# Optimization experiments

Hardware: AMD Instinct MI355X
Metric: run time of the kernel (lower is better)

## Reference

```python
import jax, jax.numpy as jnp
import numpy as np

TOP_K = 2  # num_experts_per_token


def setup_inputs() -> dict:
    key = jax.random.key(0)
    ks = jax.random.split(key, 6)
    B, S, H, F, E = 4, 2048, 1024, 4096, 8  # F = 2 * intermediate_size
    scale = 0.02
    x = jax.random.normal(ks[0], (B, S, H), dtype=jnp.float32)
    gate_w = jax.random.normal(ks[1], (E, H), dtype=jnp.float32) * scale
    w1 = jax.random.normal(ks[2], (E, H, F), dtype=jnp.float32) * scale
    b1 = jnp.zeros((E, F), dtype=jnp.float32)
    w2 = jax.random.normal(ks[3], (E, F, H), dtype=jnp.float32) * scale
    b2 = jnp.zeros((E, H), dtype=jnp.float32)
    return {"x": x, "gate_w": gate_w, "w1": w1, "b1": b1, "w2": w2, "b2": b2}


def reference(x, gate_w, w1, b1, w2, b2):
    # x: [B, S, H]; gate_w: [E, H]; w1: [E, H, F]; b1: [E, F]; w2: [E, F, H]; b2: [E, H]
    E = gate_w.shape[0]
    gate_logits = jnp.einsum('bsh,eh->bse', x, gate_w)
    gate_probs = jax.nn.softmax(gate_logits, axis=-1)
    top_v, top_i = jax.lax.top_k(gate_probs, TOP_K)  # [B, S, K]
    # Combine weight per expert: w[b,s,e] = sum_k top_v[b,s,k] * (top_i[b,s,k] == e)
    onehot = jax.nn.one_hot(top_i, E, dtype=x.dtype)          # [B, S, K, E]
    comb_w = jnp.einsum('bsk,bske->bse', top_v, onehot)       # [B, S, E]
    out = jnp.zeros_like(x)
    for e in range(E):  # small fixed expert loop
        h = jax.nn.silu(jnp.einsum('bsh,hf->bsf', x, w1[e]) + b1[e])
        y = jnp.einsum('bsf,fh->bsh', h, w2[e]) + b2[e]
        out = out + y * comb_w[..., e:e + 1]
    return out
```

## Files before the change

kernel.cpp:

```cpp
#include <hip/hip_runtime.h>
#include <stdint.h>

#define T_TOK 8192
#define HDIM  1024
#define FDIM  4096
#define NEXP  8
#define BT    256
#define RCAP  (2*T_TOK + NEXP*256)
#define LDSB  65536

typedef short  short8  __attribute__((ext_vector_type(8)));
typedef unsigned short ushort8 __attribute__((ext_vector_type(8)));
typedef float  f32x4   __attribute__((ext_vector_type(4)));

#define MFMA __builtin_amdgcn_mfma_f32_16x16x32_bf16

__device__ __forceinline__ unsigned short f2bf(float f) {
  unsigned u = __float_as_uint(f);
  u += 0x7fffu + ((u >> 16) & 1u);
  return (unsigned short)(u >> 16);
}
__device__ __forceinline__ float bf2f(unsigned short u) {
  return __uint_as_float((unsigned)u << 16);
}

__device__ __forceinline__ void gload16(const void* g, void* l) {
  __builtin_amdgcn_global_load_lds(
      (const __attribute__((address_space(1))) void*)g,
      (__attribute__((address_space(3))) void*)l, 16, 0, 0);
}

__device__ __forceinline__ const short8* lds_frag(const char* base, int row, int kbyte) {
  int b = row * 128 + kbyte;
  b ^= ((b >> 9) & 1) << 5;
  return (const short8*)(base + b);
}

__global__ void k_convert_x(const float* __restrict__ x, unsigned short* __restrict__ xb) {
  int i = (blockIdx.x * 256 + threadIdx.x) * 4;
  float4 v = *(const float4*)(x + i);
  ushort4 o;
  o.x = f2bf(v.x); o.y = f2bf(v.y); o.z = f2bf(v.z); o.w = f2bf(v.w);
  *(ushort4*)(xb + i) = o;
}

__global__ __launch_bounds__(256) void k_transp_cvt(const float* __restrict__ in,
                                                    unsigned short* __restrict__ out,
                                                    int K, int N) {
  __shared__ unsigned short s[64][72];
  const float* ine = in + (size_t)blockIdx.z * K * N;
  unsigned short* oute = out + (size_t)blockIdx.z * K * N;
  int k0 = blockIdx.y * 64, n0 = blockIdx.x * 64;
  int t = threadIdx.x;
  int kr = t >> 4, nc = (t & 15) * 4;
#pragma unroll
  for (int it = 0; it < 4; ++it) {
    int k = it * 16 + kr;
    float4 v = *(const float4*)(ine + (size_t)(k0 + k) * N + n0 + nc);
    ushort4 u = make_ushort4(f2bf(v.x), f2bf(v.y), f2bf(v.z), f2bf(v.w));
    *(ushort4*)(&s[k][nc]) = u;
  }
  __syncthreads();
  int nr = t >> 3, kc = (t & 7) * 8;
#pragma unroll
  for (int v = 0; v < 2; ++v) {
    int n = v * 32 + nr;
    ushort8 o;
#pragma unroll
    for (int j = 0; j < 8; ++j) o[j] = s[kc + j][n];
    *(ushort8*)(oute + (size_t)(n0 + n) * K + k0 + kc) = o;
  }
}

__global__ void k_gate(const float* __restrict__ x, const float* __restrict__ gw,
                       int2* __restrict__ eidx, float2* __restrict__ ewt) {
  int tid = threadIdx.x;
  int lane = tid & 63;
  int t = blockIdx.x * 4 + (tid >> 6);
  const float* xr = x + (size_t)t * HDIM;
  float acc[NEXP];
#pragma unroll
  for (int e = 0; e < NEXP; e++) acc[e] = 0.f;
#pragma unroll
  for (int i = 0; i < HDIM / 64; i++) {
    float xv = xr[i * 64 + lane];
#pragma unroll
    for (int e = 0; e < NEXP; e++) acc[e] += xv * gw[e * HDIM + i * 64 + lane];
  }
#pragma unroll
  for (int e = 0; e < NEXP; e++) {
    acc[e] += __shfl_xor(acc[e], 32);
    acc[e] += __shfl_xor(acc[e], 16);
    acc[e] += __shfl_xor(acc[e], 8);
    acc[e] += __shfl_xor(acc[e], 4);
    acc[e] += __shfl_xor(acc[e], 2);
    acc[e] += __shfl_xor(acc[e], 1);
  }
  float m = acc[0];
#pragma unroll
  for (int e = 1; e < NEXP; e++) m = fmaxf(m, acc[e]);
  float p[NEXP]; float s = 0.f;
#pragma unroll
  for (int e = 0; e < NEXP; e++) { p[e] = expf(acc[e] - m); s += p[e]; }
  float inv = 1.f / s;
#pragma unroll
  for (int e = 0; e < NEXP; e++) p[e] *= inv;
  int b0 = 0; float v0 = p[0];
#pragma unroll
  for (int e = 1; e < NEXP; e++) if (p[e] > v0) { v0 = p[e]; b0 = e; }
  int b1i = (b0 == 0) ? 1 : 0; float v1 = p[b1i];
#pragma unroll
  for (int e = 0; e < NEXP; e++) if (e != b0 && p[e] > v1) { v1 = p[e]; b1i = e; }
  if (lane == 0) { eidx[t] = make_int2(b0, b1i); ewt[t] = make_float2(v0, v1); }
}

__global__ void k_compact(const int2* __restrict__ eidx,
                          int* __restrict__ list_tok, int* __restrict__ counts) {
  int e = blockIdx.x;
  int tid = threadIdx.x, lane = tid & 63, wid = tid >> 6;
  __shared__ int sbase;
  __shared__ int wcnt[4];
  if (tid == 0) sbase = 0;
  __syncthreads();
  for (int c = 0; c < T_TOK; c += 256) {
    int t = c + tid;
    int2 ei = eidx[t];
    bool sel = (ei.x == e) || (ei.y == e);
    unsigned long long b = __ballot(sel);
    if (lane == 0) wcnt[wid] = __popcll(b);
    __syncthreads();
    int pre = sbase;
    for (int w = 0; w < wid; w++) pre += wcnt[w];
    int pos = pre + __popcll(b & ((1ull << lane) - 1ull));
    if (sel) list_tok[e * T_TOK + pos] = t;
    __syncthreads();
    if (tid == 0) sbase += wcnt[0] + wcnt[1] + wcnt[2] + wcnt[3];
    __syncthreads();
  }
  if (tid == 0) counts[e] = sbase;
}

__global__ void k_offsets(const int* __restrict__ counts, int* __restrict__ off_pad) {
  if (threadIdx.x == 0) {
    int o = 0;
    off_pad[0] = 0;
    for (int e = 0; e < NEXP; e++) {
      o += ((counts[e] + BT - 1) / BT) * BT;
      off_pad[e + 1] = o;
    }
  }
}

__global__ void k_invert(const int* __restrict__ list_tok, const int* __restrict__ counts,
                         const int* __restrict__ off_pad, const int2* __restrict__ eidx,
                         int2* __restrict__ tok2slot) {
  int e = blockIdx.y;
  int p = blockIdx.x * 256 + threadIdx.x;
  if (p < counts[e]) {
    int t = list_tok[e * T_TOK + p];
    int slot = off_pad[e] + p;
    if (eidx[t].x == e) tok2slot[t].x = slot;
    else                tok2slot[t].y = slot;
  }
}

#define STAGE_A(u_, v_) { \
    char* lb_ = smem + (((v_)&1) ? LDSB : 0) + (u_)*16384; \
    gload16(gA[u_][0] + (size_t)(v_)*128, lb_ + dst0); \
    gload16(gA[u_][1] + (size_t)(v_)*128, lb_ + dst1); }
#define STAGE_B(u_, v_) { \
    char* lb_ = smem + (((v_)&1) ? LDSB : 0) + 32768 + (u_)*16384; \
    gload16(gB[u_][0] + (size_t)(v_)*128, lb_ + dst0); \
    gload16(gB[u_][1] + (size_t)(v_)*128, lb_ + dst1); }

#define PHASE(MA, MB, STAGE_STMT, TAIL_STMT) { \
    short8 aA0 = *lds_frag(rdA, (MA)*16 + lr, g16); \
    short8 aA1 = *lds_frag(rdA, (MA)*16 + lr, 64 + g16); \
    short8 aB0 = *lds_frag(rdA, (MB)*16 + lr, g16); \
    short8 aB1 = *lds_frag(rdA, (MB)*16 + lr, 64 + g16); \
    STAGE_STMT; \
    __builtin_amdgcn_s_barrier(); \
    asm volatile("s_waitcnt lgkmcnt(0)" ::: "memory"); \
    __builtin_amdgcn_sched_barrier(0); \
    __builtin_amdgcn_s_setprio(1); \
    acc[MA][0] = MFMA(aA0, b00, acc[MA][0], 0,0,0); acc[MA][0] = MFMA(aA1, b01, acc[MA][0], 0,0,0); \
    acc[MA][1] = MFMA(aA0, b10, acc[MA][1], 0,0,0); acc[MA][1] = MFMA(aA1, b11, acc[MA][1], 0,0,0); \
    acc[MA][2] = MFMA(aA0, b20, acc[MA][2], 0,0,0); acc[MA][2] = MFMA(aA1, b21, acc[MA][2], 0,0,0); \
    acc[MA][3] = MFMA(aA0, b30, acc[MA][3], 0,0,0); acc[MA][3] = MFMA(aA1, b31, acc[MA][3], 0,0,0); \
    acc[MB][0] = MFMA(aB0, b00, acc[MB][0], 0,0,0); acc[MB][0] = MFMA(aB1, b01, acc[MB][0], 0,0,0); \
    acc[MB][1] = MFMA(aB0, b10, acc[MB][1], 0,0,0); acc[MB][1] = MFMA(aB1, b11, acc[MB][1], 0,0,0); \
    acc[MB][2] = MFMA(aB0, b20, acc[MB][2], 0,0,0); acc[MB][2] = MFMA(aB1, b21, acc[MB][2], 0,0,0); \
    acc[MB][3] = MFMA(aB0, b30, acc[MB][3], 0,0,0); acc[MB][3] = MFMA(aB1, b31, acc[MB][3], 0,0,0); \
    __builtin_amdgcn_s_setprio(0); \
    TAIL_STMT; \
    __builtin_amdgcn_s_barrier(); }

#define READ_B4 \
    short8 b00 = *lds_frag(rdB, rb +      lr, g16), b01 = *lds_frag(rdB, rb +      lr, 64 + g16); \
    short8 b10 = *lds_frag(rdB, rb + 16 + lr, g16), b11 = *lds_frag(rdB, rb + 16 + lr, 64 + g16); \
    short8 b20 = *lds_frag(rdB, rb + 32 + lr, g16), b21 = *lds_frag(rdB, rb + 32 + lr, 64 + g16); \
    short8 b30 = *lds_frag(rdB, rb + 48 + lr, g16), b31 = *lds_frag(rdB, rb + 48 + lr, 64 + g16);

#define GEMM_TILE_LOOP(NT) \
  STAGE_A(0,0); STAGE_A(1,0); STAGE_B(0,0); STAGE_B(1,0); STAGE_B(0,1); STAGE_B(1,1); \
  asm volatile("s_waitcnt vmcnt(4)" ::: "memory"); \
  __builtin_amdgcn_s_barrier(); \
  for (int v = 0; v < (NT); ++v) { \
    const char* rdA = smem + ((v&1) ? LDSB : 0) + wm * 16384; \
    const char* rdB = smem + ((v&1) ? LDSB : 0) + 32768 + (wn >> 1) * 16384; \
    int rb = (wn & 1) * 64; \
    READ_B4; \
    PHASE(0, 1, { if (v+1 < (NT)) STAGE_A(0, v+1); }, {}); \
    PHASE(2, 3, { if (v+1 < (NT)) STAGE_A(1, v+1); }, {}); \
    PHASE(4, 5, { if (v+2 < (NT)) STAGE_B(0, v+2); }, {}); \
    PHASE(6, 7, { if (v+2 < (NT)) STAGE_B(1, v+2); }, { \
      if (v+2 < (NT))      { asm volatile("s_waitcnt vmcnt(4)" ::: "memory"); } \
      else if (v+1 < (NT)) { asm volatile("s_waitcnt vmcnt(0)" ::: "memory"); } }); \
  }

__global__ __launch_bounds__(512, 2) void k_gemm1(
    const unsigned short* __restrict__ xb, const unsigned short* __restrict__ w1t,
    const float* __restrict__ b1, const int* __restrict__ list_tok,
    const int* __restrict__ counts, const int* __restrict__ off_pad,
    unsigned short* __restrict__ h) {
  extern __shared__ char smem[];
  int bid = blockIdx.x;
  int wl = (bid & 7) * 144 + (bid >> 3);
  int r0 = (wl >> 4) * BT;
  int n0 = (wl & 15) * BT;
  if (r0 >= off_pad[NEXP]) return;
  int e = 0;
#pragma unroll
  for (int i = 0; i < NEXP; ++i) if (r0 >= off_pad[i + 1]) e = i + 1;
  int base = off_pad[e], cnt = counts[e];

  int t = threadIdx.x, l = t & 63, w = t >> 6;
  int wm = w >> 2, wn = w & 3;
  int lr = l & 15, g16 = (l >> 4) * 16;

  int dst0 = t * 16, dst1 = t * 16 + 8192;
  int srow = t >> 3;
  int skb = ((t & 7) * 16) ^ (((t >> 5) & 1) << 5);
  const char* gA[2][2];
  const char* gB[2][2];
#pragma unroll
  for (int u = 0; u < 2; ++u)
#pragma unroll
    for (int j = 0; j < 2; ++j) {
      int row = u * 128 + srow + 64 * j;
      int se = r0 - base + row;
      int tok = (se < cnt) ? list_tok[e * T_TOK + se] : 0;
      gA[u][j] = (const char*)(xb + (size_t)tok * HDIM) + skb;
      gB[u][j] = (const char*)(w1t + (size_t)e * FDIM * HDIM + (size_t)(n0 + row) * HDIM) + skb;
    }

  f32x4 acc[8][4];
#pragma unroll
  for (int m = 0; m < 8; ++m)
#pragma unroll
    for (int n = 0; n < 4; ++n) acc[m][n] = (f32x4){0.f, 0.f, 0.f, 0.f};

  GEMM_TILE_LOOP(HDIM / 64);

  const float* b1e = b1 + (size_t)e * FDIM + n0;
  unsigned short* Cs = (unsigned short*)smem;
  int lh4 = (l >> 4) * 4;
#pragma unroll
  for (int n = 0; n < 4; ++n) {
    int col = wn * 64 + n * 16 + lr;
    float bv = b1e[col];
#pragma unroll
    for (int m = 0; m < 8; ++m) {
      int row = wm * 128 + m * 16 + lh4;
#pragma unroll
      for (int i = 0; i < 4; ++i) {
        float vv = acc[m][n][i] + bv;
        Cs[(size_t)(row + i) * BT + col] = f2bf(vv / (1.f + __expf(-vv)));
      }
    }
  }
  __syncthreads();
#pragma unroll
  for (int s = 0; s < 16; ++s) {
    int lin = s * 512 + t;
    int row = lin >> 5, c8 = (lin & 31) * 8;
    *(ushort8*)(h + (size_t)(r0 + row) * FDIM + n0 + c8) = *(const ushort8*)(Cs + (size_t)row * BT + c8);
  }
}

__global__ __launch_bounds__(512, 2) void k_gemm2(
    const unsigned short* __restrict__ h, const unsigned short* __restrict__ w2t,
    const float* __restrict__ b2, const int* __restrict__ off_pad,
    unsigned short* __restrict__ ypart) {
  extern __shared__ char smem[];
  int bid = blockIdx.x;
  int wl = (bid & 7) * 36 + (bid >> 3);
  int r0 = (wl >> 2) * BT;
  int n0 = (wl & 3) * BT;
  if (r0 >= off_pad[NEXP]) return;
  int e = 0;
#pragma unroll
  for (int i = 0; i < NEXP; ++i) if (r0 >= off_pad[i + 1]) e = i + 1;

  int t = threadIdx.x, l = t & 63, w = t >> 6;
  int wm = w >> 2, wn = w & 3;
  int lr = l & 15, g16 = (l >> 4) * 16;

  int dst0 = t * 16, dst1 = t * 16 + 8192;
  int srow = t >> 3;
  int skb = ((t & 7) * 16) ^ (((t >> 5) & 1) << 5);
  const char* gA[2][2];
  const char* gB[2][2];
#pragma unroll
  for (int u = 0; u < 2; ++u)
#pragma unroll
    for (int j = 0; j < 2; ++j) {
      int row = u * 128 + srow + 64 * j;
      gA[u][j] = (const char*)(h + (size_t)(r0 + row) * FDIM) + skb;
      gB[u][j] = (const char*)(w2t + (size_t)e * HDIM * FDIM + (size_t)(n0 + row) * FDIM) + skb;
    }

  f32x4 acc[8][4];
#pragma unroll
  for (int m = 0; m < 8; ++m)
#pragma unroll
    for (int n = 0; n < 4; ++n) acc[m][n] = (f32x4){0.f, 0.f, 0.f, 0.f};

  GEMM_TILE_LOOP(FDIM / 64);

  const float* b2e = b2 + (size_t)e * HDIM + n0;
  unsigned short* Cs = (unsigned short*)smem;
  int lh4 = (l >> 4) * 4;
#pragma unroll
  for (int n = 0; n < 4; ++n) {
    int col = wn * 64 + n * 16 + lr;
    float bv = b2e[col];
#pragma unroll
    for (int m = 0; m < 8; ++m) {
      int row = wm * 128 + m * 16 + lh4;
#pragma unroll
      for (int i = 0; i < 4; ++i)
        Cs[(size_t)(row + i) * BT + col] = f2bf(acc[m][n][i] + bv);
    }
  }
  __syncthreads();
#pragma unroll
  for (int s = 0; s < 16; ++s) {
    int lin = s * 512 + t;
    int row = lin >> 5, c8 = (lin & 31) * 8;
    *(ushort8*)(ypart + (size_t)(r0 + row) * HDIM + n0 + c8) = *(const ushort8*)(Cs + (size_t)row * BT + c8);
  }
}

__global__ void k_reduce(const unsigned short* __restrict__ ypart,
                         const int2* __restrict__ tok2slot, const float2* __restrict__ ewt,
                         float* __restrict__ out) {
  int idx = blockIdx.x * 256 + threadIdx.x;
  int t = idx >> 7;
  int c8 = (idx & 127) * 8;
  int2 s = tok2slot[t];
  float2 wv = ewt[t];
  ushort8 a = *(const ushort8*)(ypart + (size_t)s.x * HDIM + c8);
  ushort8 b = *(const ushort8*)(ypart + (size_t)s.y * HDIM + c8);
  float o[8];
#pragma unroll
  for (int j = 0; j < 8; ++j) o[j] = wv.x * bf2f((unsigned short)a[j]) + wv.y * bf2f((unsigned short)b[j]);
  float* op = out + (size_t)t * HDIM + c8;
  *(float4*)op = make_float4(o[0], o[1], o[2], o[3]);
  *(float4*)(op + 4) = make_float4(o[4], o[5], o[6], o[7]);
}

extern "C" void kernel_launch(void* const* d_in, const int* in_sizes, int n_in,
                              void* d_out, int out_size, void* d_ws, size_t ws_size,
                              hipStream_t stream) {
  const float* x  = (const float*)d_in[0];
  const float* gw = (const float*)d_in[1];
  const float* w1 = (const float*)d_in[2];
  const float* b1 = (const float*)d_in[3];
  const float* w2 = (const float*)d_in[4];
  const float* b2 = (const float*)d_in[5];
  float* out = (float*)d_out;

  char* ws = (char*)d_ws;
  size_t off = 0;
  unsigned short* xb = (unsigned short*)(ws + off); off += (size_t)T_TOK * HDIM * 2;
  int2*   eidx = (int2*)(ws + off);   off += (size_t)T_TOK * 8;
  float2* ewt  = (float2*)(ws + off); off += (size_t)T_TOK * 8;
  int2* tok2slot = (int2*)(ws + off); off += (size_t)T_TOK * 8;
  int*  list_tok = (int*)(ws + off);  off += (size_t)NEXP * T_TOK * 4;
  int* counts  = (int*)(ws + off); off += 64;
  int* off_pad = (int*)(ws + off); off += 64;
  off = (off + 255) & ~(size_t)255;
  unsigned short* h     = (unsigned short*)(ws + off); off += (size_t)RCAP * FDIM * 2;
  unsigned short* wT    = (unsigned short*)(ws + off); off += (size_t)NEXP * HDIM * FDIM * 2;
  unsigned short* ypart = (unsigned short*)(ws + off); off += (size_t)RCAP * HDIM * 2;
  if (ws_size < off) return;

  hipFuncSetAttribute((const void*)k_gemm1, hipFuncAttributeMaxDynamicSharedMemorySize, 131072);
  hipFuncSetAttribute((const void*)k_gemm2, hipFuncAttributeMaxDynamicSharedMemorySize, 131072);

  k_convert_x<<<T_TOK * HDIM / 1024, 256, 0, stream>>>(x, xb);
  k_gate<<<T_TOK / 4, 256, 0, stream>>>(x, gw, eidx, ewt);
  k_compact<<<NEXP, 256, 0, stream>>>(eidx, list_tok, counts);
  k_offsets<<<1, 64, 0, stream>>>(counts, off_pad);
  k_invert<<<dim3(T_TOK / 256, NEXP), 256, 0, stream>>>(list_tok, counts, off_pad, eidx, tok2slot);
  k_transp_cvt<<<dim3(FDIM / 64, HDIM / 64, NEXP), 256, 0, stream>>>(w1, wT, HDIM, FDIM);
  k_gemm1<<<8 * 144, 512, 131072, stream>>>(xb, wT, b1, list_tok, counts, off_pad, h);
  k_transp_cvt<<<dim3(HDIM / 64, FDIM / 64, NEXP), 256, 0, stream>>>(w2, wT, FDIM, HDIM);
  k_gemm2<<<8 * 36, 512, 131072, stream>>>(h, wT, b2, off_pad, ypart);
  k_reduce<<<T_TOK * (HDIM / 8) / 256, 256, 0, stream>>>(ypart, tok2slot, ewt, out);
}
```

Baseline: 564.4 us.

## Split-K gemm2 into two halves, fuse x conversion into gate, new LDS swizzle

Three changes. gemm2 is split along K into two halves that write separate bf16 partial buffers, with the bias added only in the first half, and the reduce kernel sums both halves. This doubles the gemm2 grid from 288 to 576 blocks to fill more CUs, at the cost of extra partial-output traffic and reads. The x-to-bf16 conversion is folded into the gate kernel, which removes one launch and one read of x. The LDS XOR swizzle also changes to a full 8-way row-based pattern to cut bank conflicts on fragment reads.

Measured after the change: 523.0 us. 7.3% less time.

```diff
diff --git a/kernel.cpp b/kernel.cpp
--- a/kernel.cpp
+++ b/kernel.cpp
@@ -31,17 +31,8 @@
 }
 
 __device__ __forceinline__ const short8* lds_frag(const char* base, int row, int kbyte) {
-  int b = row * 128 + kbyte;
-  b ^= ((b >> 9) & 1) << 5;
+  int b = row * 128 + (kbyte ^ ((row & 7) << 4));
   return (const short8*)(base + b);
-}
-
-__global__ void k_convert_x(const float* __restrict__ x, unsigned short* __restrict__ xb) {
-  int i = (blockIdx.x * 256 + threadIdx.x) * 4;
-  float4 v = *(const float4*)(x + i);
-  ushort4 o;
-  o.x = f2bf(v.x); o.y = f2bf(v.y); o.z = f2bf(v.z); o.w = f2bf(v.w);
-  *(ushort4*)(xb + i) = o;
 }
 
 __global__ __launch_bounds__(256) void k_transp_cvt(const float* __restrict__ in,
@@ -73,17 +64,20 @@
 }
 
 __global__ void k_gate(const float* __restrict__ x, const float* __restrict__ gw,
+                       unsigned short* __restrict__ xb,
                        int2* __restrict__ eidx, float2* __restrict__ ewt) {
   int tid = threadIdx.x;
   int lane = tid & 63;
   int t = blockIdx.x * 4 + (tid >> 6);
   const float* xr = x + (size_t)t * HDIM;
+  unsigned short* xbr = xb + (size_t)t * HDIM;
   float acc[NEXP];
 #pragma unroll
   for (int e = 0; e < NEXP; e++) acc[e] = 0.f;
 #pragma unroll
   for (int i = 0; i < HDIM / 64; i++) {
     float xv = xr[i * 64 + lane];
+    xbr[i * 64 + lane] = f2bf(xv);
 #pragma unroll
     for (int e = 0; e < NEXP; e++) acc[e] += xv * gw[e * HDIM + i * 64 + lane];
   }
@@ -240,7 +234,7 @@
 
   int dst0 = t * 16, dst1 = t * 16 + 8192;
   int srow = t >> 3;
-  int skb = ((t & 7) * 16) ^ (((t >> 5) & 1) << 5);
+  int skb = (((t & 7) ^ ((t >> 3) & 7)) << 4);
   const char* gA[2][2];
   const char* gB[2][2];
 #pragma unroll
@@ -291,12 +285,14 @@
 __global__ __launch_bounds__(512, 2) void k_gemm2(
     const unsigned short* __restrict__ h, const unsigned short* __restrict__ w2t,
     const float* __restrict__ b2, const int* __restrict__ off_pad,
-    unsigned short* __restrict__ ypart) {
+    unsigned short* __restrict__ ypartA, unsigned short* __restrict__ ypartB) {
   extern __shared__ char smem[];
   int bid = blockIdx.x;
-  int wl = (bid & 7) * 36 + (bid >> 3);
-  int r0 = (wl >> 2) * BT;
-  int n0 = (wl & 3) * BT;
+  int wl = (bid & 7) * 72 + (bid >> 3);
+  int mB = wl >> 3, rem = wl & 7;
+  int r0 = mB * BT;
+  int n0 = (rem >> 1) * BT;
+  int z  = rem & 1;
   if (r0 >= off_pad[NEXP]) return;
   int e = 0;
 #pragma unroll
@@ -308,7 +304,7 @@
 
   int dst0 = t * 16, dst1 = t * 16 + 8192;
   int srow = t >> 3;
-  int skb = ((t & 7) * 16) ^ (((t >> 5) & 1) << 5);
+  int skb = (((t & 7) ^ ((t >> 3) & 7)) << 4);
   const char* gA[2][2];
   const char* gB[2][2];
 #pragma unroll
@@ -316,8 +312,8 @@
 #pragma unroll
     for (int j = 0; j < 2; ++j) {
       int row = u * 128 + srow + 64 * j;
-      gA[u][j] = (const char*)(h + (size_t)(r0 + row) * FDIM) + skb;
-      gB[u][j] = (const char*)(w2t + (size_t)e * HDIM * FDIM + (size_t)(n0 + row) * FDIM) + skb;
+      gA[u][j] = (const char*)(h + (size_t)(r0 + row) * FDIM + (size_t)z * 2048) + skb;
+      gB[u][j] = (const char*)(w2t + (size_t)e * HDIM * FDIM + (size_t)(n0 + row) * FDIM + (size_t)z * 2048) + skb;
     }
 
   f32x4 acc[8][4];
@@ -326,15 +322,16 @@
 #pragma unroll
     for (int n = 0; n < 4; ++n) acc[m][n] = (f32x4){0.f, 0.f, 0.f, 0.f};
 
-  GEMM_TILE_LOOP(FDIM / 64);
+  GEMM_TILE_LOOP(2048 / 64);
 
   const float* b2e = b2 + (size_t)e * HDIM + n0;
+  unsigned short* yp = z ? ypartB : ypartA;
   unsigned short* Cs = (unsigned short*)smem;
   int lh4 = (l >> 4) * 4;
 #pragma unroll
   for (int n = 0; n < 4; ++n) {
     int col = wn * 64 + n * 16 + lr;
-    float bv = b2e[col];
+    float bv = (z == 0) ? b2e[col] : 0.f;
 #pragma unroll
     for (int m = 0; m < 8; ++m) {
       int row = wm * 128 + m * 16 + lh4;
@@ -348,11 +345,12 @@
   for (int s = 0; s < 16; ++s) {
     int lin = s * 512 + t;
     int row = lin >> 5, c8 = (lin & 31) * 8;
-    *(ushort8*)(ypart + (size_t)(r0 + row) * HDIM + n0 + c8) = *(const ushort8*)(Cs + (size_t)row * BT + c8);
-  }
-}
-
-__global__ void k_reduce(const unsigned short* __restrict__ ypart,
+    *(ushort8*)(yp + (size_t)(r0 + row) * HDIM + n0 + c8) = *(const ushort8*)(Cs + (size_t)row * BT + c8);
+  }
+}
+
+__global__ void k_reduce(const unsigned short* __restrict__ ypartA,
+                         const unsigned short* __restrict__ ypartB,
                          const int2* __restrict__ tok2slot, const float2* __restrict__ ewt,
                          float* __restrict__ out) {
   int idx = blockIdx.x * 256 + threadIdx.x;
@@ -360,11 +358,15 @@
   int c8 = (idx & 127) * 8;
   int2 s = tok2slot[t];
   float2 wv = ewt[t];
-  ushort8 a = *(const ushort8*)(ypart + (size_t)s.x * HDIM + c8);
-  ushort8 b = *(const ushort8*)(ypart + (size_t)s.y * HDIM + c8);
+  ushort8 a0 = *(const ushort8*)(ypartA + (size_t)s.x * HDIM + c8);
+  ushort8 a1 = *(const ushort8*)(ypartB + (size_t)s.x * HDIM + c8);
+  ushort8 b0 = *(const ushort8*)(ypartA + (size_t)s.y * HDIM + c8);
+  ushort8 b1 = *(const ushort8*)(ypartB + (size_t)s.y * HDIM + c8);
   float o[8];
 #pragma unroll
-  for (int j = 0; j < 8; ++j) o[j] = wv.x * bf2f((unsigned short)a[j]) + wv.y * bf2f((unsigned short)b[j]);
+  for (int j = 0; j < 8; ++j)
+    o[j] = wv.x * (bf2f((unsigned short)a0[j]) + bf2f((unsigned short)a1[j]))
+         + wv.y * (bf2f((unsigned short)b0[j]) + bf2f((unsigned short)b1[j]));
   float* op = out + (size_t)t * HDIM + c8;
   *(float4*)op = make_float4(o[0], o[1], o[2], o[3]);
   *(float4*)(op + 4) = make_float4(o[4], o[5], o[6], o[7]);
@@ -391,22 +393,22 @@
   int* counts  = (int*)(ws + off); off += 64;
   int* off_pad = (int*)(ws + off); off += 64;
   off = (off + 255) & ~(size_t)255;
-  unsigned short* h     = (unsigned short*)(ws + off); off += (size_t)RCAP * FDIM * 2;
-  unsigned short* wT    = (unsigned short*)(ws + off); off += (size_t)NEXP * HDIM * FDIM * 2;
-  unsigned short* ypart = (unsigned short*)(ws + off); off += (size_t)RCAP * HDIM * 2;
+  unsigned short* h      = (unsigned short*)(ws + off); off += (size_t)RCAP * FDIM * 2;
+  unsigned short* wT     = (unsigned short*)(ws + off); off += (size_t)NEXP * HDIM * FDIM * 2;
+  unsigned short* ypartA = (unsigned short*)(ws + off); off += (size_t)RCAP * HDIM * 2;
+  unsigned short* ypartB = (unsigned short*)(ws + off); off += (size_t)RCAP * HDIM * 2;
   if (ws_size < off) return;
 
   hipFuncSetAttribute((const void*)k_gemm1, hipFuncAttributeMaxDynamicSharedMemorySize, 131072);
   hipFuncSetAttribute((const void*)k_gemm2, hipFuncAttributeMaxDynamicSharedMemorySize, 131072);
 
-  k_convert_x<<<T_TOK * HDIM / 1024, 256, 0, stream>>>(x, xb);
-  k_gate<<<T_TOK / 4, 256, 0, stream>>>(x, gw, eidx, ewt);
+  k_gate<<<T_TOK / 4, 256, 0, stream>>>(x, gw, xb, eidx, ewt);
   k_compact<<<NEXP, 256, 0, stream>>>(eidx, list_tok, counts);
   k_offsets<<<1, 64, 0, stream>>>(counts, off_pad);
   k_invert<<<dim3(T_TOK / 256, NEXP), 256, 0, stream>>>(list_tok, counts, off_pad, eidx, tok2slot);
   k_transp_cvt<<<dim3(FDIM / 64, HDIM / 64, NEXP), 256, 0, stream>>>(w1, wT, HDIM, FDIM);
   k_gemm1<<<8 * 144, 512, 131072, stream>>>(xb, wT, b1, list_tok, counts, off_pad, h);
   k_transp_cvt<<<dim3(HDIM / 64, FDIM / 64, NEXP), 256, 0, stream>>>(w2, wT, FDIM, HDIM);
-  k_gemm2<<<8 * 36, 512, 131072, stream>>>(h, wT, b2, off_pad, ypart);
-  k_reduce<<<T_TOK * (HDIM / 8) / 256, 256, 0, stream>>>(ypart, tok2slot, ewt, out);
-}
+  k_gemm2<<<8 * 72, 512, 131072, stream>>>(h, wT, b2, off_pad, ypartA, ypartB);
+  k_reduce<<<T_TOK * (HDIM / 8) / 256, 256, 0, stream>>>(ypartA, ypartB, tok2slot, ewt, out);
+}
```
